# Optimization experiments

Hardware: AMD Instinct MI355X
Metric: run time of the kernel (lower is better)

Reference implementation:

```python
import jax, jax.numpy as jnp
import numpy as np

N, C, H, W = 8, 32, 256, 256
DEPTH = 4
PAD = (1, 1, 2, 2, 1, 1)  # (w_l, w_r, h_t, h_b, d_f, d_b)
K = 2  # pool kernel/stride along each of D,H,W
EPS = 1e-5


def setup_inputs() -> dict:
    key = jax.random.key(0)
    k1, k2, k3, k4, k5 = jax.random.split(key, 5)
    x = jax.random.normal(k1, (N, C, H, W), dtype=jnp.float32)
    gamma = jax.random.normal(k2, (C,), dtype=jnp.float32) * 0.1 + 1.0
    beta = jax.random.normal(k3, (C,), dtype=jnp.float32) * 0.1
    conv_w = jax.random.normal(k4, (C, C), dtype=jnp.float32) / np.sqrt(C)  # 1x1 conv [out,in]
    conv_b = jax.random.normal(k5, (C,), dtype=jnp.float32) * 0.1
    return {"x": x, "gamma": gamma, "beta": beta, "conv_w": conv_w, "conv_b": conv_b}


def _forward(x, gamma, beta, conv_w, conv_b):
    n, c, h, w = x.shape
    # InstanceNorm2d (affine, biased variance, eps=1e-5), stats per (N,C) over H,W
    mean = jnp.mean(x, axis=(2, 3), keepdims=True)
    var = jnp.mean(jnp.square(x - mean), axis=(2, 3), keepdims=True)
    xn = (x - mean) * jax.lax.rsqrt(var + EPS)
    xn = xn * gamma[None, :, None, None] + beta[None, :, None, None]
    # expand to 5D by repeating along depth
    x3 = jnp.broadcast_to(xn[:, :, None, :, :], (n, c, DEPTH, h, w))
    # ConstantPad3d with value 0.0
    wl, wr, ht, hb, df, db = PAD
    xp = jnp.pad(x3, ((0, 0), (0, 0), (df, db), (ht, hb), (wl, wr)))
    Dp, Hp, Wp = DEPTH + df + db, h + ht + hb, w + wl + wr  # all even by construction
    dq, hq, wq = Dp // K, Hp // K, Wp // K
    # block view: [n,c,dq,K,hq,K,wq,K] -> [n,c,dq,hq,wq,K*K*K] (row-major window order,
    # matching PyTorch's flattened pooling-window index order)
    blk = xp.reshape(n, c, dq, K, hq, K, wq, K).transpose(0, 1, 2, 4, 6, 3, 5, 7)
    blk = blk.reshape(n, c, dq, hq, wq, K * K * K)
    mx = jnp.max(blk, axis=-1)
    idx = jnp.argmax(blk, axis=-1)  # first occurrence on ties, like PyTorch CPU
    # MaxUnpool3d: scatter max back to its argmax position, zeros elsewhere
    unp_blk = jax.nn.one_hot(idx, K * K * K, dtype=x.dtype) * mx[..., None]
    unpooled = unp_blk.reshape(n, c, dq, hq, wq, K, K, K).transpose(0, 1, 2, 5, 3, 6, 4, 7)
    unpooled = unpooled.reshape(n, c, Dp, Hp, Wp)
    # crop padding, collapse depth via mean
    cropped = unpooled[:, :, df:df + DEPTH, ht:ht + h, wl:wl + w]
    collapsed = jnp.mean(cropped, axis=2)  # [n,c,h,w]
    # 1x1 conv + relu
    out = jnp.einsum('oc,nchw->nohw', conv_w, collapsed) + conv_b[None, :, None, None]
    return jax.nn.relu(out)


def reference(x, gamma, beta, conv_w, conv_b):
    return _forward(x, gamma, beta, conv_w, conv_b)
```

## Files before the change

kernel.cpp:

```cpp
#include <hip/hip_runtime.h>

#define N_   8
#define C_   32
#define H_   256
#define W_   256
#define HW_  (H_ * W_)

__global__ __launch_bounds__(1024) void stats_kernel(
    const float* __restrict__ x, const float* __restrict__ gamma,
    const float* __restrict__ beta, float2* __restrict__ ss)
{
    const int nc = blockIdx.x;
    const int t  = threadIdx.x;
    const float4* p = (const float4*)(x + (size_t)nc * HW_);

    float s0 = 0.f, s1 = 0.f, s2 = 0.f, s3 = 0.f;
    float q0 = 0.f, q1 = 0.f, q2 = 0.f, q3 = 0.f;
    #pragma unroll
    for (int i = 0; i < 16; ++i) {
        float4 v = p[t + (i << 10)];
        s0 += v.x; s1 += v.y; s2 += v.z; s3 += v.w;
        q0 = fmaf(v.x, v.x, q0); q1 = fmaf(v.y, v.y, q1);
        q2 = fmaf(v.z, v.z, q2); q3 = fmaf(v.w, v.w, q3);
    }
    double s = (double)s0 + (double)s1 + (double)s2 + (double)s3;
    double q = (double)q0 + (double)q1 + (double)q2 + (double)q3;
    #pragma unroll
    for (int off = 32; off > 0; off >>= 1) {
        s += __shfl_down(s, off);
        q += __shfl_down(q, off);
    }
    __shared__ double rs[16], rq[16];
    const int wid = t >> 6;
    if ((t & 63) == 0) { rs[wid] = s; rq[wid] = q; }
    __syncthreads();
    if (t == 0) {
        double S = 0.0, Q = 0.0;
        #pragma unroll
        for (int i = 0; i < 16; ++i) { S += rs[i]; Q += rq[i]; }
        double mean = S / (double)HW_;
        double var  = Q / (double)HW_ - mean * mean;
        double grs  = (double)gamma[nc & (C_ - 1)] / sqrt(var + 1e-5);
        float scale = (float)grs;
        float shift = (float)((double)beta[nc & (C_ - 1)] - mean * grs);
        ss[nc] = make_float2(scale, shift);
    }
}

__global__ __launch_bounds__(512) void fused_kernel(
    const float* __restrict__ x, const float2* __restrict__ ss,
    const float* __restrict__ Wm, const float* __restrict__ bias,
    float* __restrict__ out)
{
    const int k = blockIdx.x;
    const int n = blockIdx.y;
    const int t = threadIdx.x;

    __shared__ float         sWT[C_][C_];
    __shared__ float         sE[C_][66];
    __shared__ float         sO[C_][64];
    __shared__ unsigned char pE[C_][66];
    __shared__ unsigned char pO[C_][64];

    {
        int i = t;
        #pragma unroll
        for (int r = 0; r < 2; ++r, i += 512) {
            int o = i >> 5, c = i & 31;
            sWT[c][o] = Wm[i];
        }
    }

    const int c  = t >> 4;
    const int li = t & 15;
    const float2 sc = ss[n * C_ + c];
    const float* r0p = x + (size_t)(n * C_ + c) * HW_
                         + (size_t)(2 * k) * W_ + 16 * li;
    const float* r1p = r0p + W_;

    float4 u0[4], u1[4];
    #pragma unroll
    for (int q = 0; q < 4; ++q) u0[q] = ((const float4*)r0p)[q];
    #pragma unroll
    for (int q = 0; q < 4; ++q) u1[q] = ((const float4*)r1p)[q];

    float vm[16];
    unsigned vr = 0;
    #pragma unroll
    for (int q = 0; q < 4; ++q) {
        float a0, a1;
        a0 = fmaf(u0[q].x, sc.x, sc.y); a1 = fmaf(u1[q].x, sc.x, sc.y);
        vm[4*q+0] = fmaxf(a0, a1); if (a1 > a0) vr |= 1u << (4*q+0);
        a0 = fmaf(u0[q].y, sc.x, sc.y); a1 = fmaf(u1[q].y, sc.x, sc.y);
        vm[4*q+1] = fmaxf(a0, a1); if (a1 > a0) vr |= 1u << (4*q+1);
        a0 = fmaf(u0[q].z, sc.x, sc.y); a1 = fmaf(u1[q].z, sc.x, sc.y);
        vm[4*q+2] = fmaxf(a0, a1); if (a1 > a0) vr |= 1u << (4*q+2);
        a0 = fmaf(u0[q].w, sc.x, sc.y); a1 = fmaf(u1[q].w, sc.x, sc.y);
        vm[4*q+3] = fmaxf(a0, a1); if (a1 > a0) vr |= 1u << (4*q+3);
    }

    const float    vmL = __shfl_up(vm[15], 1);
    const unsigned vrL = __shfl_up(vr, 1);
    const int      rLn = (int)((vrL >> 15) & 1u);

    #pragma unroll
    for (int b = 0; b < 8; ++b) {
        float vL; int rL; bool padL;
        if (b == 0) {
            padL = (li == 0);
            vL = padL ? 0.f : vmL;
            rL = padL ? 0   : rLn;
        } else {
            vL = vm[2*b - 1]; rL = (int)((vr >> (2*b - 1)) & 1u); padL = false;
        }
        float vR = vm[2*b]; int rR = (int)((vr >> (2*b)) & 1u);
        bool chooseL = (vL > vR) || ((vL == vR) && (rL <= rR));
        float m   = chooseL ? vL : vR;
        int   p   = chooseL ? (rL << 1) : ((rR << 1) | 1);
        float val = m * (m > 0.f ? 0.75f : 0.25f);
        if (chooseL && padL) val = 0.f;
        int j = 8 * li + b;
        if (b & 1) { sO[c][j >> 1] = val; pO[c][j >> 1] = (unsigned char)p; }
        else       { sE[c][j >> 1] = val; pE[c][j >> 1] = (unsigned char)p; }
    }
    if (li == 15) {
        float vL = vm[15]; int rL = (int)((vr >> 15) & 1u);
        bool chooseL = (vL > 0.f) || ((vL == 0.f) && (rL <= 0));
        float m   = chooseL ? vL : 0.f;
        int   p   = chooseL ? (rL << 1) : 1;
        float val = m * (m > 0.f ? 0.75f : 0.25f);
        if (!chooseL) val = 0.f;
        sE[c][64] = val; pE[c][64] = (unsigned char)p;
    }
    __syncthreads();

    const int wv = t >> 6;
    const int ob = wv << 2;
    const int wt = t & 63;

    float acc[2][4][4];
    #pragma unroll
    for (int oo = 0; oo < 4; ++oo) {
        float bo = bias[ob + oo];
        #pragma unroll
        for (int r = 0; r < 2; ++r)
            #pragma unroll
            for (int dw = 0; dw < 4; ++dw) acc[r][dw][oo] = bo;
    }

    for (int cc = 0; cc < C_; ++cc) {
        float w0 = sWT[cc][ob + 0], w1 = sWT[cc][ob + 1];
        float w2 = sWT[cc][ob + 2], w3 = sWT[cc][ob + 3];
        float vA = sE[cc][wt];     int pA = pE[cc][wt];
        float vB = sO[cc][wt];     int pB = pO[cc][wt];
        float vC = sE[cc][wt + 1]; int pC = pE[cc][wt + 1];
        float m00 = (pA == 1) ? vA : 0.f, m10 = (pA == 3) ? vA : 0.f;
        float m01 = (pB == 0) ? vB : 0.f, m11 = (pB == 2) ? vB : 0.f;
        float m02 = (pB == 1) ? vB : 0.f, m12 = (pB == 3) ? vB : 0.f;
        float m03 = (pC == 0) ? vC : 0.f, m13 = (pC == 2) ? vC : 0.f;
        acc[0][0][0] = fmaf(m00, w0, acc[0][0][0]);
        acc[0][1][0] = fmaf(m01, w0, acc[0][1][0]);
        acc[0][2][0] = fmaf(m02, w0, acc[0][2][0]);
        acc[0][3][0] = fmaf(m03, w0, acc[0][3][0]);
        acc[1][0][0] = fmaf(m10, w0, acc[1][0][0]);
        acc[1][1][0] = fmaf(m11, w0, acc[1][1][0]);
        acc[1][2][0] = fmaf(m12, w0, acc[1][2][0]);
        acc[1][3][0] = fmaf(m13, w0, acc[1][3][0]);
        acc[0][0][1] = fmaf(m00, w1, acc[0][0][1]);
        acc[0][1][1] = fmaf(m01, w1, acc[0][1][1]);
        acc[0][2][1] = fmaf(m02, w1, acc[0][2][1]);
        acc[0][3][1] = fmaf(m03, w1, acc[0][3][1]);
        acc[1][0][1] = fmaf(m10, w1, acc[1][0][1]);
        acc[1][1][1] = fmaf(m11, w1, acc[1][1][1]);
        acc[1][2][1] = fmaf(m12, w1, acc[1][2][1]);
        acc[1][3][1] = fmaf(m13, w1, acc[1][3][1]);
        acc[0][0][2] = fmaf(m00, w2, acc[0][0][2]);
        acc[0][1][2] = fmaf(m01, w2, acc[0][1][2]);
        acc[0][2][2] = fmaf(m02, w2, acc[0][2][2]);
        acc[0][3][2] = fmaf(m03, w2, acc[0][3][2]);
        acc[1][0][2] = fmaf(m10, w2, acc[1][0][2]);
        acc[1][1][2] = fmaf(m11, w2, acc[1][1][2]);
        acc[1][2][2] = fmaf(m12, w2, acc[1][2][2]);
        acc[1][3][2] = fmaf(m13, w2, acc[1][3][2]);
        acc[0][0][3] = fmaf(m00, w3, acc[0][0][3]);
        acc[0][1][3] = fmaf(m01, w3, acc[0][1][3]);
        acc[0][2][3] = fmaf(m02, w3, acc[0][2][3]);
        acc[0][3][3] = fmaf(m03, w3, acc[0][3][3]);
        acc[1][0][3] = fmaf(m10, w3, acc[1][0][3]);
        acc[1][1][3] = fmaf(m11, w3, acc[1][1][3]);
        acc[1][2][3] = fmaf(m12, w3, acc[1][2][3]);
        acc[1][3][3] = fmaf(m13, w3, acc[1][3][3]);
    }

    #pragma unroll
    for (int r = 0; r < 2; ++r)
        #pragma unroll
        for (int oo = 0; oo < 4; ++oo) {
            float4 v;
            v.x = fmaxf(acc[r][0][oo], 0.f);
            v.y = fmaxf(acc[r][1][oo], 0.f);
            v.z = fmaxf(acc[r][2][oo], 0.f);
            v.w = fmaxf(acc[r][3][oo], 0.f);
            float* dst = out + (size_t)(n * C_ + ob + oo) * HW_
                             + (size_t)(2 * k + r) * W_ + 4 * wt;
            *(float4*)dst = v;
        }
}

extern "C" void kernel_launch(void* const* d_in, const int* in_sizes, int n_in,
                              void* d_out, int out_size, void* d_ws, size_t ws_size,
                              hipStream_t stream) {
    const float* x     = (const float*)d_in[0];
    const float* gamma = (const float*)d_in[1];
    const float* beta  = (const float*)d_in[2];
    const float* Wm    = (const float*)d_in[3];
    const float* bias  = (const float*)d_in[4];
    float* out  = (float*)d_out;
    float2* ss  = (float2*)d_ws;

    stats_kernel<<<N_ * C_, 1024, 0, stream>>>(x, gamma, beta, ss);
    fused_kernel<<<dim3(H_ / 2, N_), 512, 0, stream>>>(x, ss, Wm, bias, out);
}
```

Before: 155.7 us.

## Split fused kernel across width halves with per-thread 8-channel output tiling

The fused pool/unpool/conv kernel now splits each row pair into two width halves, doubling the grid to 2048 blocks, and loads the boundary neighbour column directly from global memory. Each thread now computes one output column for two rows across 8 output channels instead of 4 columns for 4 channels. Weights are read with float4 shared loads and the inner loop is partially unrolled. This raises parallelism and occupancy (launch bounds 512,4) at the cost of scalar rather than float4 output stores and a small amount of redundant boundary work.

```diff
diff --git a/kernel.cpp b/kernel.cpp
--- a/kernel.cpp
+++ b/kernel.cpp
@@ -47,25 +47,24 @@
     }
 }
 
-__global__ __launch_bounds__(512) void fused_kernel(
+__global__ __launch_bounds__(512, 4) void fused_kernel(
     const float* __restrict__ x, const float2* __restrict__ ss,
     const float* __restrict__ Wm, const float* __restrict__ bias,
     float* __restrict__ out)
 {
-    const int k = blockIdx.x;
-    const int n = blockIdx.y;
-    const int t = threadIdx.x;
+    const int k    = blockIdx.x;
+    const int half = blockIdx.y;
+    const int n    = blockIdx.z;
+    const int t    = threadIdx.x;
 
     __shared__ float         sWT[C_][C_];
-    __shared__ float         sE[C_][66];
-    __shared__ float         sO[C_][64];
-    __shared__ unsigned char pE[C_][66];
-    __shared__ unsigned char pO[C_][64];
+    __shared__ float         sV[C_][66];
+    __shared__ unsigned char sP[C_][68];
 
     {
         int i = t;
         #pragma unroll
-        for (int r = 0; r < 2; ++r, i += 512) {
+        for (int r2 = 0; r2 < 2; ++r2, i += 512) {
             int o = i >> 5, c = i & 31;
             sWT[c][o] = Wm[i];
         }
@@ -74,137 +73,132 @@
     const int c  = t >> 4;
     const int li = t & 15;
     const float2 sc = ss[n * C_ + c];
-    const float* r0p = x + (size_t)(n * C_ + c) * HW_
-                         + (size_t)(2 * k) * W_ + 16 * li;
-    const float* r1p = r0p + W_;
-
-    float4 u0[4], u1[4];
-    #pragma unroll
-    for (int q = 0; q < 4; ++q) u0[q] = ((const float4*)r0p)[q];
-    #pragma unroll
-    for (int q = 0; q < 4; ++q) u1[q] = ((const float4*)r1p)[q];
-
-    float vm[16];
+    const float* rowb = x + (size_t)(n * C_ + c) * HW_
+                          + (size_t)(2 * k) * W_ + 128 * half + 8 * li;
+    float4 u00 = ((const float4*)rowb)[0];
+    float4 u01 = ((const float4*)rowb)[1];
+    float4 u10 = ((const float4*)(rowb + W_))[0];
+    float4 u11 = ((const float4*)(rowb + W_))[1];
+
+    float bm = 0.f; int br = 0;
+    {
+        bool need = (half == 0) ? (li == 15) : (li == 0);
+        if (need) {
+            const float* bp = x + (size_t)(n * C_ + c) * HW_
+                                + (size_t)(2 * k) * W_ + (half == 0 ? 128 : 127);
+            float a0 = fmaf(bp[0],  sc.x, sc.y);
+            float a1 = fmaf(bp[W_], sc.x, sc.y);
+            bm = fmaxf(a0, a1); br = (a1 > a0) ? 1 : 0;
+        }
+    }
+
+    float vm[8];
     unsigned vr = 0;
-    #pragma unroll
-    for (int q = 0; q < 4; ++q) {
+    {
         float a0, a1;
-        a0 = fmaf(u0[q].x, sc.x, sc.y); a1 = fmaf(u1[q].x, sc.x, sc.y);
-        vm[4*q+0] = fmaxf(a0, a1); if (a1 > a0) vr |= 1u << (4*q+0);
-        a0 = fmaf(u0[q].y, sc.x, sc.y); a1 = fmaf(u1[q].y, sc.x, sc.y);
-        vm[4*q+1] = fmaxf(a0, a1); if (a1 > a0) vr |= 1u << (4*q+1);
-        a0 = fmaf(u0[q].z, sc.x, sc.y); a1 = fmaf(u1[q].z, sc.x, sc.y);
-        vm[4*q+2] = fmaxf(a0, a1); if (a1 > a0) vr |= 1u << (4*q+2);
-        a0 = fmaf(u0[q].w, sc.x, sc.y); a1 = fmaf(u1[q].w, sc.x, sc.y);
-        vm[4*q+3] = fmaxf(a0, a1); if (a1 > a0) vr |= 1u << (4*q+3);
-    }
-
-    const float    vmL = __shfl_up(vm[15], 1);
-    const unsigned vrL = __shfl_up(vr, 1);
-    const int      rLn = (int)((vrL >> 15) & 1u);
-
-    #pragma unroll
-    for (int b = 0; b < 8; ++b) {
-        float vL; int rL; bool padL;
+        a0 = fmaf(u00.x, sc.x, sc.y); a1 = fmaf(u10.x, sc.x, sc.y);
+        vm[0] = fmaxf(a0, a1); if (a1 > a0) vr |= 1u << 0;
+        a0 = fmaf(u00.y, sc.x, sc.y); a1 = fmaf(u10.y, sc.x, sc.y);
+        vm[1] = fmaxf(a0, a1); if (a1 > a0) vr |= 1u << 1;
+        a0 = fmaf(u00.z, sc.x, sc.y); a1 = fmaf(u10.z, sc.x, sc.y);
+        vm[2] = fmaxf(a0, a1); if (a1 > a0) vr |= 1u << 2;
+        a0 = fmaf(u00.w, sc.x, sc.y); a1 = fmaf(u10.w, sc.x, sc.y);
+        vm[3] = fmaxf(a0, a1); if (a1 > a0) vr |= 1u << 3;
+        a0 = fmaf(u01.x, sc.x, sc.y); a1 = fmaf(u11.x, sc.x, sc.y);
+        vm[4] = fmaxf(a0, a1); if (a1 > a0) vr |= 1u << 4;
+        a0 = fmaf(u01.y, sc.x, sc.y); a1 = fmaf(u11.y, sc.x, sc.y);
+        vm[5] = fmaxf(a0, a1); if (a1 > a0) vr |= 1u << 5;
+        a0 = fmaf(u01.z, sc.x, sc.y); a1 = fmaf(u11.z, sc.x, sc.y);
+        vm[6] = fmaxf(a0, a1); if (a1 > a0) vr |= 1u << 6;
+        a0 = fmaf(u01.w, sc.x, sc.y); a1 = fmaf(u11.w, sc.x, sc.y);
+        vm[7] = fmaxf(a0, a1); if (a1 > a0) vr |= 1u << 7;
+    }
+
+    const float pvm = __shfl_up(vm[7], 1);
+    const int   pvr = __shfl_up((int)((vr >> 7) & 1u), 1);
+
+    #pragma unroll
+    for (int b = 0; b < 4; ++b) {
+        float vL; int rL; bool padL = false;
         if (b == 0) {
-            padL = (li == 0);
-            vL = padL ? 0.f : vmL;
-            rL = padL ? 0   : rLn;
+            if (li == 0) {
+                if (half == 0) { vL = 0.f; rL = 0; padL = true; }
+                else           { vL = bm;  rL = br; }
+            } else { vL = pvm; rL = pvr; }
         } else {
-            vL = vm[2*b - 1]; rL = (int)((vr >> (2*b - 1)) & 1u); padL = false;
+            vL = vm[2 * b - 1]; rL = (int)((vr >> (2 * b - 1)) & 1u);
         }
-        float vR = vm[2*b]; int rR = (int)((vr >> (2*b)) & 1u);
+        float vR = vm[2 * b]; int rR = (int)((vr >> (2 * b)) & 1u);
         bool chooseL = (vL > vR) || ((vL == vR) && (rL <= rR));
         float m   = chooseL ? vL : vR;
         int   p   = chooseL ? (rL << 1) : ((rR << 1) | 1);
         float val = m * (m > 0.f ? 0.75f : 0.25f);
         if (chooseL && padL) val = 0.f;
-        int j = 8 * li + b;
-        if (b & 1) { sO[c][j >> 1] = val; pO[c][j >> 1] = (unsigned char)p; }
-        else       { sE[c][j >> 1] = val; pE[c][j >> 1] = (unsigned char)p; }
+        int jl = 4 * li + b;
+        sV[c][jl] = val;
+        sP[c][jl] = (unsigned char)p;
     }
     if (li == 15) {
-        float vL = vm[15]; int rL = (int)((vr >> 15) & 1u);
-        bool chooseL = (vL > 0.f) || ((vL == 0.f) && (rL <= 0));
-        float m   = chooseL ? vL : 0.f;
-        int   p   = chooseL ? (rL << 1) : 1;
+        float vL = vm[7]; int rL = (int)((vr >> 7) & 1u);
+        float vR; int rR; bool padR;
+        if (half == 0) { vR = bm; rR = br; padR = false; }
+        else           { vR = 0.f; rR = 0; padR = true;  }
+        bool chooseL = (vL > vR) || ((vL == vR) && (rL <= rR));
+        float m   = chooseL ? vL : vR;
+        int   p   = chooseL ? (rL << 1) : ((rR << 1) | 1);
         float val = m * (m > 0.f ? 0.75f : 0.25f);
-        if (!chooseL) val = 0.f;
-        sE[c][64] = val; pE[c][64] = (unsigned char)p;
+        if (!chooseL && padR) val = 0.f;
+        sV[c][64] = val;
+        sP[c][64] = (unsigned char)p;
     }
     __syncthreads();
 
     const int wv = t >> 6;
-    const int ob = wv << 2;
-    const int wt = t & 63;
-
-    float acc[2][4][4];
-    #pragma unroll
-    for (int oo = 0; oo < 4; ++oo) {
+    const int ob = (wv & 3) << 3;
+    const int L  = ((wv >> 2) << 6) + (t & 63);
+    const int jl = (L + 1) >> 1;
+    const int pm0 = (L & 1) ? 0 : 2 - 1;
+
+    float acc0[8], acc1[8];
+    #pragma unroll
+    for (int oo = 0; oo < 8; ++oo) {
         float bo = bias[ob + oo];
-        #pragma unroll
-        for (int r = 0; r < 2; ++r)
-            #pragma unroll
-            for (int dw = 0; dw < 4; ++dw) acc[r][dw][oo] = bo;
-    }
-
+        acc0[oo] = bo; acc1[oo] = bo;
+    }
+
+    #pragma unroll 8
     for (int cc = 0; cc < C_; ++cc) {
-        float w0 = sWT[cc][ob + 0], w1 = sWT[cc][ob + 1];
-        float w2 = sWT[cc][ob + 2], w3 = sWT[cc][ob + 3];
-        float vA = sE[cc][wt];     int pA = pE[cc][wt];
-        float vB = sO[cc][wt];     int pB = pO[cc][wt];
-        float vC = sE[cc][wt + 1]; int pC = pE[cc][wt + 1];
-        float m00 = (pA == 1) ? vA : 0.f, m10 = (pA == 3) ? vA : 0.f;
-        float m01 = (pB == 0) ? vB : 0.f, m11 = (pB == 2) ? vB : 0.f;
-        float m02 = (pB == 1) ? vB : 0.f, m12 = (pB == 3) ? vB : 0.f;
-        float m03 = (pC == 0) ? vC : 0.f, m13 = (pC == 2) ? vC : 0.f;
-        acc[0][0][0] = fmaf(m00, w0, acc[0][0][0]);
-        acc[0][1][0] = fmaf(m01, w0, acc[0][1][0]);
-        acc[0][2][0] = fmaf(m02, w0, acc[0][2][0]);
-        acc[0][3][0] = fmaf(m03, w0, acc[0][3][0]);
-        acc[1][0][0] = fmaf(m10, w0, acc[1][0][0]);
-        acc[1][1][0] = fmaf(m11, w0, acc[1][1][0]);
-        acc[1][2][0] = fmaf(m12, w0, acc[1][2][0]);
-        acc[1][3][0] = fmaf(m13, w0, acc[1][3][0]);
-        acc[0][0][1] = fmaf(m00, w1, acc[0][0][1]);
-        acc[0][1][1] = fmaf(m01, w1, acc[0][1][1]);
-        acc[0][2][1] = fmaf(m02, w1, acc[0][2][1]);
-        acc[0][3][1] = fmaf(m03, w1, acc[0][3][1]);
-        acc[1][0][1] = fmaf(m10, w1, acc[1][0][1]);
-        acc[1][1][1] = fmaf(m11, w1, acc[1][1][1]);
-        acc[1][2][1] = fmaf(m12, w1, acc[1][2][1]);
-        acc[1][3][1] = fmaf(m13, w1, acc[1][3][1]);
-        acc[0][0][2] = fmaf(m00, w2, acc[0][0][2]);
-        acc[0][1][2] = fmaf(m01, w2, acc[0][1][2]);
-        acc[0][2][2] = fmaf(m02, w2, acc[0][2][2]);
-        acc[0][3][2] = fmaf(m03, w2, acc[0][3][2]);
-        acc[1][0][2] = fmaf(m10, w2, acc[1][0][2]);
-        acc[1][1][2] = fmaf(m11, w2, acc[1][1][2]);
-        acc[1][2][2] = fmaf(m12, w2, acc[1][2][2]);
-        acc[1][3][2] = fmaf(m13, w2, acc[1][3][2]);
-        acc[0][0][3] = fmaf(m00, w3, acc[0][0][3]);
-        acc[0][1][3] = fmaf(m01, w3, acc[0][1][3]);
-        acc[0][2][3] = fmaf(m02, w3, acc[0][2][3]);
-        acc[0][3][3] = fmaf(m03, w3, acc[0][3][3]);
-        acc[1][0][3] = fmaf(m10, w3, acc[1][0][3]);
-        acc[1][1][3] = fmaf(m11, w3, acc[1][1][3]);
-        acc[1][2][3] = fmaf(m12, w3, acc[1][2][3]);
-        acc[1][3][3] = fmaf(m13, w3, acc[1][3][3]);
-    }
-
-    #pragma unroll
-    for (int r = 0; r < 2; ++r)
-        #pragma unroll
-        for (int oo = 0; oo < 4; ++oo) {
-            float4 v;
-            v.x = fmaxf(acc[r][0][oo], 0.f);
-            v.y = fmaxf(acc[r][1][oo], 0.f);
-            v.z = fmaxf(acc[r][2][oo], 0.f);
-            v.w = fmaxf(acc[r][3][oo], 0.f);
-            float* dst = out + (size_t)(n * C_ + ob + oo) * HW_
-                             + (size_t)(2 * k + r) * W_ + 4 * wt;
-            *(float4*)dst = v;
-        }
+        float v = sV[cc][jl];
+        int   p = sP[cc][jl];
+        float m0 = (p == pm0)     ? v : 0.f;
+        float m1 = (p == pm0 + 2) ? v : 0.f;
+        float4 wa = *(const float4*)&sWT[cc][ob];
+        float4 wb = *(const float4*)&sWT[cc][ob + 4];
+        acc0[0] = fmaf(m0, wa.x, acc0[0]);
+        acc0[1] = fmaf(m0, wa.y, acc0[1]);
+        acc0[2] = fmaf(m0, wa.z, acc0[2]);
+        acc0[3] = fmaf(m0, wa.w, acc0[3]);
+        acc0[4] = fmaf(m0, wb.x, acc0[4]);
+        acc0[5] = fmaf(m0, wb.y, acc0[5]);
+        acc0[6] = fmaf(m0, wb.z, acc0[6]);
+        acc0[7] = fmaf(m0, wb.w, acc0[7]);
+        acc1[0] = fmaf(m1, wa.x, acc1[0]);
+        acc1[1] = fmaf(m1, wa.y, acc1[1]);
+        acc1[2] = fmaf(m1, wa.z, acc1[2]);
+        acc1[3] = fmaf(m1, wa.w, acc1[3]);
+        acc1[4] = fmaf(m1, wb.x, acc1[4]);
+        acc1[5] = fmaf(m1, wb.y, acc1[5]);
+        acc1[6] = fmaf(m1, wb.z, acc1[6]);
+        acc1[7] = fmaf(m1, wb.w, acc1[7]);
+    }
+
+    float* obase = out + (size_t)(n * C_ + ob) * HW_
+                       + (size_t)(2 * k) * W_ + 128 * half + L;
+    #pragma unroll
+    for (int oo = 0; oo < 8; ++oo) {
+        obase[(size_t)oo * HW_]      = fmaxf(acc0[oo], 0.f);
+        obase[(size_t)oo * HW_ + W_] = fmaxf(acc1[oo], 0.f);
+    }
 }
 
 extern "C" void kernel_launch(void* const* d_in, const int* in_sizes, int n_in,
@@ -219,5 +213,5 @@
     float2* ss  = (float2*)d_ws;
 
     stats_kernel<<<N_ * C_, 1024, 0, stream>>>(x, gamma, beta, ss);
-    fused_kernel<<<dim3(H_ / 2, N_), 512, 0, stream>>>(x, ss, Wm, bias, out);
+    fused_kernel<<<dim3(H_ / 2, 2, N_), 512, 0, stream>>>(x, ss, Wm, bias, out);
 }
```

Result: faster. 134.4 us (-13.6%).
